# Kernel tuning notes

Measured on AMD Instinct MI355X. Metric: run time of the kernel, lower is better.

Reference implementation:

```python
import jax, jax.numpy as jnp
import numpy as np

N_Q = 5000
MEM = 50
KDIM = 50
VDIM = 200
FC = 50
B = 2048
S = 200


def setup_inputs() -> dict:
    key = jax.random.key(0)
    ks = jax.random.split(key, 14)
    inp = {}
    inp["q_data"] = jax.random.randint(ks[0], (B, S), 0, N_Q, dtype=jnp.int64)
    inp["qa_data"] = jax.random.randint(ks[1], (B, S), 0, 2 * N_Q, dtype=jnp.int64)
    # learned parameters (kaiming-ish random init)
    inp["q_embed_w"] = jax.random.normal(ks[2], (N_Q + 1, KDIM), jnp.float32) * 0.2
    inp["qa_embed_w"] = jax.random.normal(ks[3], (2 * N_Q + 1, VDIM), jnp.float32) * 0.1
    inp["key_memory"] = jax.random.normal(ks[4], (MEM, KDIM), jnp.float32) * 0.2
    inp["init_value_memory"] = jax.random.normal(ks[5], (MEM, VDIM), jnp.float32) * 0.1
    # DKVMN write gates: erase (sigmoid) and add (tanh) transforms of qa embedding
    inp["erase_w"] = jax.random.normal(ks[6], (VDIM, VDIM), jnp.float32) * 0.1
    inp["erase_b"] = jnp.zeros((VDIM,), jnp.float32)
    inp["add_w"] = jax.random.normal(ks[7], (VDIM, VDIM), jnp.float32) * 0.1
    inp["add_b"] = jnp.zeros((VDIM,), jnp.float32)
    # prediction MLP: Linear(VDIM+KDIM -> FC), Tanh, Linear(FC -> 1)
    inp["pred_w1"] = jax.random.normal(ks[8], (VDIM + KDIM, FC), jnp.float32) * 0.1
    inp["pred_b1"] = jnp.zeros((FC,), jnp.float32)
    inp["pred_w2"] = jax.random.normal(ks[9], (FC, 1), jnp.float32) * 0.2
    inp["pred_b2"] = jnp.zeros((1,), jnp.float32)
    return inp


def _dkvmn_forward(q_data, qa_data, q_embed_w, qa_embed_w, key_memory,
                   init_value_memory, erase_w, erase_b, add_w, add_b,
                   pred_w1, pred_b1, pred_w2, pred_b2):
    q_emb = q_embed_w[q_data]    # [B, S, KDIM]
    qa_emb = qa_embed_w[qa_data]  # [B, S, VDIM]
    batch = q_data.shape[0]
    Mv0 = jnp.broadcast_to(init_value_memory, (batch, MEM, VDIM))

    def step(Mv, xs):
        q_t, qa_t = xs  # [B, KDIM], [B, VDIM]
        # attention over memory slots
        w = jax.nn.softmax(q_t @ key_memory.T, axis=-1)          # [B, MEM]
        read = jnp.einsum('bm,bmv->bv', w, Mv)                    # [B, VDIM]
        h = jnp.tanh(jnp.concatenate([read, q_t], -1) @ pred_w1 + pred_b1)
        p = jax.nn.sigmoid((h @ pred_w2 + pred_b2)[:, 0])         # [B]
        # erase/add write
        e = jax.nn.sigmoid(qa_t @ erase_w + erase_b)              # [B, VDIM]
        a = jnp.tanh(qa_t @ add_w + add_b)                        # [B, VDIM]
        Mv_new = Mv * (1.0 - w[:, :, None] * e[:, None, :]) + w[:, :, None] * a[:, None, :]
        return Mv_new, p

    xs = (jnp.swapaxes(q_emb, 0, 1), jnp.swapaxes(qa_emb, 0, 1))  # time-major
    _, preds = jax.lax.scan(step, Mv0, xs)                        # [S, B]
    return preds.T                                                # [B, S]


def reference(q_data, qa_data, q_embed_w, qa_embed_w, key_memory,
              init_value_memory, erase_w, erase_b, add_w, add_b,
              pred_w1, pred_b1, pred_w2, pred_b2):
    preds = _dkvmn_forward(q_data, qa_data, q_embed_w, qa_embed_w, key_memory,
                           init_value_memory, erase_w, erase_b, add_w, add_b,
                           pred_w1, pred_b1, pred_w2, pred_b2)
    zeros = jnp.zeros_like(preds)
    return (preds, zeros, zeros, zeros)
```

## Files before the change

### kernel.cpp

```cpp
#include <hip/hip_runtime.h>
#include <hip/hip_fp16.h>


#define NQ1   5001
#define NQA   10001
#define MEMN  50
#define KD    50
#define VD    200
#define FC    50
#define BB    2048
#define SS    200
#define EA_R  16
#define WHS   32

#define EA_B   626
#define WQ_B   1251
#define PACK_B 8
#define PREP_G (EA_B + WQ_B + PACK_B)

typedef unsigned int   u32;
typedef unsigned short u16;
typedef short    s8v __attribute__((ext_vector_type(8)));
typedef float    f4v __attribute__((ext_vector_type(4)));
typedef _Float16 h2v __attribute__((ext_vector_type(2)));
typedef u32      u4v __attribute__((ext_vector_type(4)));

__device__ __forceinline__ float fast_sigmoid(float x) { return 1.f / (1.f + __expf(-x)); }
__device__ __forceinline__ float fast_tanh(float x) {
    float e2 = __expf(2.f * x);
    return 1.f - 2.f / (e2 + 1.f);
}
__device__ __forceinline__ float bfu16_to_f(u16 u) {
    union { float f; u32 i; } x; x.i = ((u32)u) << 16; return x.f;
}
__device__ __forceinline__ u16 f_to_bfu16(float f) {
    union { float f; u32 i; } x; x.f = f;
    return (u16)((x.i + 0x7fffu + ((x.i >> 16) & 1u)) >> 16);
}
__device__ __forceinline__ h2v u32_to_h2v(u32 u) {
    union { u32 i; h2v h; } x; x.i = u; return x.h;
}
__device__ __forceinline__ u16 f16bits(float f) {
    union { __half h; u16 u; } x; x.h = __float2half(f); return x.u;
}
__device__ __forceinline__ float h16_to_f(u16 u) {
    union { u16 u; __half h; } x; x.u = u; return __half2float(x.h);
}

__global__ __launch_bounds__(256) void prep(
        const float* __restrict__ qemb, const float* __restrict__ km,
        const float* __restrict__ w1,   const float* __restrict__ b1,
        const float* __restrict__ qaemb,
        const float* __restrict__ ew,   const float* __restrict__ ebias,
        const float* __restrict__ aw,   const float* __restrict__ abias,
        float* __restrict__ Wt, u32* __restrict__ Wh, float* __restrict__ Q1,
        u32* __restrict__ EA, u16* __restrict__ W1s,
        float* __restrict__ out_aux) {
    const int tid = threadIdx.x;
    const int blk = blockIdx.x;

    for (size_t i = (size_t)blk * 256 + tid; i < 3ull * BB * SS;
         i += (size_t)PREP_G * 256)
        out_aux[i] = 0.f;

    __shared__ float smem[VD * EA_R];

    if (blk < EA_B) {
        const int r0 = blk * EA_R;
        if (tid < VD) {
            #pragma unroll
            for (int r = 0; r < EA_R; ++r) {
                int row = r0 + r;
                smem[tid * EA_R + r] = (row < NQA) ? qaemb[(size_t)row * VD + tid] : 0.f;
            }
        }
        __syncthreads();
        if (tid >= VD) return;

        float accE[EA_R], accA[EA_R];
        #pragma unroll
        for (int r = 0; r < EA_R; ++r) { accE[r] = 0.f; accA[r] = 0.f; }
        for (int k = 0; k < VD; ++k) {
            float we = ew[k * VD + tid];
            float wa = aw[k * VD + tid];
            #pragma unroll
            for (int r = 0; r < EA_R; ++r) {
                float qv = smem[k * EA_R + r];
                accE[r] = fmaf(qv, we, accE[r]);
                accA[r] = fmaf(qv, wa, accA[r]);
            }
        }
        float be = ebias[tid], ba = abias[tid];
        #pragma unroll
        for (int r = 0; r < EA_R; ++r) {
            int row = r0 + r;
            if (row < NQA) {
                u16 ne16 = f16bits(-fast_sigmoid(accE[r] + be));
                u16 a16  = f16bits(fast_tanh(accA[r] + ba));
                EA[(size_t)row * VD + tid] = (u32)ne16 | ((u32)a16 << 16);
            }
        }
    } else if (blk < EA_B + WQ_B) {
        const int lane = tid & 63;
        const int wv   = tid >> 6;
        const int q    = (blk - EA_B) * 4 + wv;
        const bool qok = q < NQ1;
        float* qrow = smem + wv * 64;
        if (qok && lane < KD) qrow[lane] = qemb[q * KD + lane];
        __syncthreads();
        if (!qok) return;

        float s = -1e30f;
        if (lane < MEMN) {
            s = 0.f;
            #pragma unroll
            for (int k = 0; k < KD; ++k) s = fmaf(qrow[k], km[lane * KD + k], s);
        }
        float mx = s;
        #pragma unroll
        for (int off = 32; off >= 1; off >>= 1) mx = fmaxf(mx, __shfl_xor(mx, off, 64));
        float e = (lane < MEMN) ? __expf(s - mx) : 0.f;
        float sum = e;
        #pragma unroll
        for (int off = 32; off >= 1; off >>= 1) sum += __shfl_xor(sum, off, 64);
        float wv_ = (lane < MEMN) ? (e / sum) : 0.f;
        if (lane < MEMN) Wt[q * MEMN + lane] = wv_;

        float plo = __shfl(wv_, 2 * (lane & 31), 64);
        float phi = __shfl(wv_, 2 * (lane & 31) + 1, 64);
        if (lane < 25) {
            Wh[q * WHS + lane] = (u32)f16bits(plo) | ((u32)f16bits(phi) << 16);
        } else if (lane < WHS) {
            Wh[q * WHS + lane] = 0;
        }

        if (lane < FC) {
            float h = b1[lane];
            #pragma unroll
            for (int k = 0; k < KD; ++k)
                h = fmaf(qrow[k], w1[(VD + k) * FC + lane], h);
            Q1[q * FC + lane] = h;
        }
    } else {
        for (int idx = (blk - EA_B - WQ_B) * 256 + tid; idx < 4 * 7 * 64 * 8;
             idx += PACK_B * 256) {
            int j    = idx & 7;
            int lane = (idx >> 3) & 63;
            int kt   = (idx >> 9) % 7;
            int nt   = idx / 3584;
            int k = kt * 32 + ((lane >> 4) << 3) + j;
            int n = nt * 16 + (lane & 15);
            float v = (k < VD && n < FC) ? w1[k * FC + n] : 0.f;
            W1s[idx] = f_to_bfu16(v);
        }
    }
}

__device__ __forceinline__ void state_step_v(const u4v (&w)[6], u32 w6, u32 ea,
                                             h2v (&mv)[25], float& rdA, float& rdB) {
    h2v nev2 = u32_to_h2v(__builtin_amdgcn_perm(ea, ea, 0x01000100u));
    h2v av2  = u32_to_h2v(__builtin_amdgcn_perm(ea, ea, 0x03020302u));
    rdA = 0.f; rdB = 0.f;
    #pragma unroll
    for (int i = 0; i < 25; i += 2) {
        u32 wu0 = (i < 24) ? w[i >> 2][i & 3] : w6;
        h2v w0 = u32_to_h2v(wu0);
#if __has_builtin(__builtin_amdgcn_fdot2)
        rdA = __builtin_amdgcn_fdot2(w0, mv[i], rdA, false);
#else
        rdA = fmaf((float)w0.x, (float)mv[i].x,
              fmaf((float)w0.y, (float)mv[i].y, rdA));
#endif
        mv[i] = __builtin_elementwise_fma(
            w0, __builtin_elementwise_fma(nev2, mv[i], av2), mv[i]);
        if (i + 1 < 25) {
            h2v w1p = u32_to_h2v(w[(i + 1) >> 2][(i + 1) & 3]);
#if __has_builtin(__builtin_amdgcn_fdot2)
            rdB = __builtin_amdgcn_fdot2(w1p, mv[i + 1], rdB, false);
#else
            rdB = fmaf((float)w1p.x, (float)mv[i + 1].x,
                  fmaf((float)w1p.y, (float)mv[i + 1].y, rdB));
#endif
            mv[i + 1] = __builtin_elementwise_fma(
                w1p, __builtin_elementwise_fma(nev2, mv[i + 1], av2), mv[i + 1]);
        }
    }
}

__global__ __launch_bounds__(128) void dkvmn_state(
        const int* __restrict__ qd, const int* __restrict__ qad,
        const u32* __restrict__ Wh, const u32* __restrict__ EA,
        const float* __restrict__ ivm, u16* __restrict__ READ) {
    const int tid  = threadIdx.x;
    const int lane = tid & 63;
    const int wid  = tid >> 6;
    const int blk  = blockIdx.x;
    const int b    = blk >> 1;
    const int role = (blk & 1) * 2 + wid;
    const int base = b * SS;

    __shared__ int qs[SS], qas[SS];
    for (int i = tid; i < SS; i += 128) {
        qs[i]  = qd[base + i];
        qas[i] = qad[base + i];
    }
    __syncthreads();

    if (role < 3) {
        const int v = role * 64 + lane;

        h2v mv[25];
        #pragma unroll
        for (int i = 0; i < 25; ++i) {
            mv[i].x = (_Float16)ivm[(2 * i) * VD + v];
            mv[i].y = (_Float16)ivm[(2 * i + 1) * VD + v];
        }

        int q0  = qs[0];  asm volatile("" : "+v"(q0));
        int qw  = qs[1];  asm volatile("" : "+v"(qw));
        int qw2 = qs[2];  asm volatile("" : "+v"(qw2));
        int qa2 = qas[2];
        u32 ea_c = EA[(size_t)qas[0] * VD + v];
        u32 ea_n = EA[(size_t)qas[1] * VD + v];

        u4v wA[6]; u32 wA6;
        {
            const u32* rp = Wh + (size_t)q0 * WHS;
            #pragma unroll
            for (int j = 0; j < 6; ++j) wA[j] = *(const u4v*)(rp + j * 4);
            wA6 = rp[24];
        }

        for (int t = 0; t < SS; ++t) {
            int t3 = t + 3; t3 = (t3 < SS) ? t3 : (SS - 1);
            int qnew  = qs[t3];  asm volatile("" : "+v"(qnew));
            int qanew = qas[t3];

            u32 ea_f = EA[(size_t)qa2 * VD + v];

            float rdA, rdB;
            state_step_v(wA, wA6, ea_c, mv, rdA, rdB);
            READ[(size_t)(base + t) * VD + v] = f_to_bfu16(rdA + rdB);

            {
                const u32* rp = Wh + (size_t)qw * WHS;
                #pragma unroll
                for (int j = 0; j < 6; ++j) wA[j] = *(const u4v*)(rp + j * 4);
                wA6 = rp[24];
            }

            qw = qw2; qw2 = qnew; qa2 = qanew;
            ea_c = ea_n; ea_n = ea_f;
        }
    } else {
        const int v8  = lane & 7;
        const int grp = lane >> 3;
        const int v   = 192 + v8;

        h2v mv4[4];
        #pragma unroll
        for (int j = 0; j < 4; ++j) {
            int p = grp * 4 + j;
            if (p < 25) {
                mv4[j].x = (_Float16)ivm[(2 * p) * VD + v];
                mv4[j].y = (_Float16)ivm[(2 * p + 1) * VD + v];
            } else {
                mv4[j].x = (_Float16)0.f;
                mv4[j].y = (_Float16)0.f;
            }
        }

        int q0 = qs[0], q1 = qs[1];
        u32 ea_c = EA[(size_t)qas[0] * VD + v];
        u32 ea_n = EA[(size_t)qas[1] * VD + v];
        u4v wq_c = *(const u4v*)(Wh + (size_t)q0 * WHS + grp * 4);
        u4v wq_n = *(const u4v*)(Wh + (size_t)q1 * WHS + grp * 4);

        for (int t = 0; t < SS; ++t) {
            int tn = t + 2; tn = (tn < SS) ? tn : (SS - 1);
            int q_nn  = qs[tn];
            int qa_nn = qas[tn];
            u32 ea_nn = EA[(size_t)qa_nn * VD + v];
            u4v wq_nn = *(const u4v*)(Wh + (size_t)q_nn * WHS + grp * 4);

            h2v nev2 = u32_to_h2v(__builtin_amdgcn_perm(ea_c, ea_c, 0x01000100u));
            h2v av2  = u32_to_h2v(__builtin_amdgcn_perm(ea_c, ea_c, 0x03020302u));

            float rd = 0.f;
            #pragma unroll
            for (int j = 0; j < 4; ++j) {
                h2v w2 = u32_to_h2v(wq_c[j]);
#if __has_builtin(__builtin_amdgcn_fdot2)
                rd = __builtin_amdgcn_fdot2(w2, mv4[j], rd, false);
#else
                rd = fmaf((float)w2.x, (float)mv4[j].x,
                     fmaf((float)w2.y, (float)mv4[j].y, rd));
#endif
                mv4[j] = __builtin_elementwise_fma(
                    w2, __builtin_elementwise_fma(nev2, mv4[j], av2), mv4[j]);
            }
            rd += __shfl_xor(rd, 8, 64);
            rd += __shfl_xor(rd, 16, 64);
            rd += __shfl_xor(rd, 32, 64);
            if (grp == 0)
                READ[(size_t)(base + t) * VD + v] = f_to_bfu16(rd);

            ea_c = ea_n; ea_n = ea_nn;
            wq_c = wq_n; wq_n = wq_nn;
        }
    }
}

__global__ __launch_bounds__(256) void mlp_pred(
        const u16* __restrict__ RD, const int* __restrict__ qd,
        const float* __restrict__ Q1tab, const u16* __restrict__ W1s,
        const float* __restrict__ w2, const float* __restrict__ b2,
        float* __restrict__ out) {
    const int tid  = threadIdx.x;
    const int lane = tid & 63;
    const int wv   = tid >> 6;
    const int strip = blockIdx.x * 4 + wv;
    const int row0  = strip * 16;

    const int mrow = lane & 15;
    const int quad = lane >> 4;

    s8v a[7];
    {
        const u16* arow = RD + (size_t)(row0 + mrow) * VD + quad * 8;
        #pragma unroll
        for (int kt = 0; kt < 7; ++kt)
            a[kt] = *(const s8v*)(arow + kt * 32);
    }

    const float b2f = b2[0];
    float pf[4] = {0.f, 0.f, 0.f, 0.f};

    #pragma unroll
    for (int nt = 0; nt < 4; ++nt) {
        s8v bfr[7];
        #pragma unroll
        for (int kt = 0; kt < 7; ++kt)
            bfr[kt] = *(const s8v*)(W1s + (((nt * 7 + kt) * 64) + lane) * 8);

        f4v acc = {0.f, 0.f, 0.f, 0.f};
        #pragma unroll
        for (int kt = 0; kt < 7; ++kt)
            acc = __builtin_amdgcn_mfma_f32_16x16x32_bf16(a[kt], bfr[kt], acc, 0, 0, 0);

        const int f = nt * 16 + mrow;
        const float w2f = (f < FC) ? w2[f] : 0.f;
        #pragma unroll
        for (int r = 0; r < 4; ++r) {
            int row = row0 + quad * 4 + r;
            float h = acc[r] + Q1tab[qd[row] * FC + f];
            pf[r] = fmaf(fast_tanh(h), w2f, pf[r]);
        }
    }

    #pragma unroll
    for (int r = 0; r < 4; ++r) {
        float s = pf[r];
        s += __shfl_xor(s, 1, 64);
        s += __shfl_xor(s, 2, 64);
        s += __shfl_xor(s, 4, 64);
        s += __shfl_xor(s, 8, 64);
        if (mrow == 0)
            out[row0 + quad * 4 + r] = fast_sigmoid(s + b2f);
    }
}

__global__ void dkvmn_main(const int* __restrict__ qd, const int* __restrict__ qad,
                           const float* __restrict__ Wtab, const float* __restrict__ Q1tab,
                           const u32* __restrict__ EA,
                           const float* __restrict__ ivm,
                           const float* __restrict__ w1,
                           const float* __restrict__ w2,
                           const float* __restrict__ b2,
                           float* __restrict__ out) {
    const int tid  = threadIdx.x;
    const int b    = blockIdx.x;
    const int v    = tid;
    const int lane = tid & 63;
    const int wv   = tid >> 6;

    __shared__ alignas(16) float read_lds[4 * 52];
    __shared__ alignas(16) float part_lds[4 * 52];

    float mv[MEMN];
    if (v < VD) {
        #pragma unroll
        for (int m = 0; m < MEMN; ++m) mv[m] = ivm[m * VD + v];
    }
    float w1r[50];
    if (lane < FC) {
        #pragma unroll
        for (int i = 0; i < 50; ++i) w1r[i] = w1[(wv * 50 + i) * FC + lane];
    } else {
        #pragma unroll
        for (int i = 0; i < 50; ++i) w1r[i] = 0.f;
    }
    const float w2f = (tid < FC) ? w2[tid] : 0.f;
    const float b2f = b2[0];

    const int* qrow_i  = qd  + b * SS;
    const int* qarow_i = qad + b * SS;
    const int jchunk = v / 50;
    const int wslot  = jchunk * 52 + (v - jchunk * 50);

    for (int t = 0; t < SS; ++t) {
        const int q  = __builtin_amdgcn_readfirstlane(qrow_i[t]);
        const int qa = __builtin_amdgcn_readfirstlane(qarow_i[t]);
        const float* wrow = Wtab + q * MEMN;

        u32 ea = 0;
        if (v < VD) ea = EA[(size_t)qa * VD + v];
        float ne = h16_to_f((u16)(ea & 0xffffu));
        float av = h16_to_f((u16)(ea >> 16));

        if (v < VD) {
            float rd0 = 0.f, rd1 = 0.f;
            #pragma unroll
            for (int m = 0; m < MEMN; m += 2) {
                float wm0 = wrow[m], wm1 = wrow[m + 1];
                rd0 = fmaf(wm0, mv[m], rd0);
                mv[m] = fmaf(wm0, fmaf(ne, mv[m], av), mv[m]);
                rd1 = fmaf(wm1, mv[m + 1], rd1);
                mv[m + 1] = fmaf(wm1, fmaf(ne, mv[m + 1], av), mv[m + 1]);
            }
            read_lds[wslot] = rd0 + rd1;
        }
        __syncthreads();

        float part = 0.f;
        {
            const float* rlc = read_lds + wv * 52;
            #pragma unroll
            for (int i = 0; i < 48; i += 4) {
                float4 x = *(const float4*)(rlc + i);
                part = fmaf(x.x, w1r[i],     part);
                part = fmaf(x.y, w1r[i + 1], part);
                part = fmaf(x.z, w1r[i + 2], part);
                part = fmaf(x.w, w1r[i + 3], part);
            }
            part = fmaf(rlc[48], w1r[48], part);
            part = fmaf(rlc[49], w1r[49], part);
        }
        if (lane < FC) part_lds[wv * 52 + lane] = part;
        __syncthreads();

        if (wv == 0) {
            float pf = 0.f;
            if (lane < FC) {
                float h = part_lds[lane] + part_lds[52 + lane] +
                          part_lds[104 + lane] + part_lds[156 + lane] +
                          Q1tab[q * FC + lane];
                pf = fast_tanh(h) * w2f;
            }
            #pragma unroll
            for (int off = 32; off >= 1; off >>= 1) pf += __shfl_xor(pf, off, 64);
            if (lane == 0) out[b * SS + t] = fast_sigmoid(pf + b2f);
        }
    }
}

extern "C" void kernel_launch(void* const* d_in, const int* in_sizes, int n_in,
                              void* d_out, int out_size, void* d_ws, size_t ws_size,
                              hipStream_t stream) {
    const int* qd  = (const int*)d_in[0];
    const int* qad = (const int*)d_in[1];
    const float* qemb  = (const float*)d_in[2];
    const float* qaemb = (const float*)d_in[3];
    const float* km    = (const float*)d_in[4];
    const float* ivm   = (const float*)d_in[5];
    const float* ew    = (const float*)d_in[6];
    const float* eb    = (const float*)d_in[7];
    const float* aw    = (const float*)d_in[8];
    const float* ab    = (const float*)d_in[9];
    const float* w1    = (const float*)d_in[10];
    const float* b1    = (const float*)d_in[11];
    const float* w2    = (const float*)d_in[12];
    const float* b2    = (const float*)d_in[13];
    float* out = (float*)d_out;
    (void)in_sizes; (void)n_in; (void)out_size;

    char* ws = (char*)d_ws;
    float* Wt  = (float*)(ws);
    float* Q1  = (float*)(ws + 1000448);
    u32*   EA  = (u32*)  (ws + 2000896);
    u16*   W1s = (u16*)  (ws + 10001920);
    u32*   Wh  = (u32*)  (ws + 10034688);
    u16*   RD  = (u16*)  (ws + 10675200);
    const size_t need = 10675200ull + 163840000ull + 512ull;

    prep<<<PREP_G, 256, 0, stream>>>(qemb, km, w1, b1, qaemb, ew, eb, aw, ab,
                                     Wt, Wh, Q1, EA, W1s, out + (size_t)BB * SS);

    if (ws_size >= need) {
        dkvmn_state<<<BB * 2, 128, 0, stream>>>(qd, qad, Wh, EA, ivm, RD);
        mlp_pred<<<(BB * SS) / 64, 256, 0, stream>>>(RD, qd, Q1, W1s, w2, b2, out);
    } else {
        dkvmn_main<<<BB, 256, 0, stream>>>(qd, qad, Wt, Q1, EA, ivm, w1, w2, b2, out);
    }
}
```

Baseline: 507.3 us.

## Stage attention-weight rows into double-buffered LDS in groups of 16 steps

In the recurrent state kernel, each wave used to fetch the per-step attention-weight row from global memory, prefetching only one to two steps ahead. Now both waves of the block load the rows for the next 16 time steps into a double-buffered shared-memory tile while the current group runs. A barrier separates each group, and the inner loop reads the row from LDS. The goal is to take global-load latency off the serial time-step chain, at the cost of one block barrier per group and extra LDS traffic.

```diff
diff --git a/kernel.cpp b/kernel.cpp
--- a/kernel.cpp
+++ b/kernel.cpp
@@ -17,6 +17,9 @@
 #define WQ_B   1251
 #define PACK_B 8
 #define PREP_G (EA_B + WQ_B + PACK_B)
+
+#define WGRP  16
+#define NG    13
 
 typedef unsigned int   u32;
 typedef unsigned short u16;
@@ -200,12 +203,31 @@
     const int base = b * SS;
 
     __shared__ int qs[SS], qas[SS];
+    __shared__ u32 wlds[2][WGRP][WHS];
+
     for (int i = tid; i < SS; i += 128) {
         qs[i]  = qd[base + i];
         qas[i] = qad[base + i];
     }
     __syncthreads();
 
+    const int wword = tid & 31;
+    const int wsub  = tid >> 5;
+
+    {
+        u32 w0s[4];
+        #pragma unroll
+        for (int r = 0; r < 4; ++r) {
+            int s = r * 4 + wsub;
+            int q = qs[(s < SS) ? s : (SS - 1)];
+            w0s[r] = Wh[(size_t)q * WHS + wword];
+        }
+        #pragma unroll
+        for (int r = 0; r < 4; ++r)
+            wlds[0][r * 4 + wsub][wword] = w0s[r];
+    }
+    __syncthreads();
+
     if (role < 3) {
         const int v = role * 64 + lane;
 
@@ -216,41 +238,48 @@
             mv[i].y = (_Float16)ivm[(2 * i + 1) * VD + v];
         }
 
-        int q0  = qs[0];  asm volatile("" : "+v"(q0));
-        int qw  = qs[1];  asm volatile("" : "+v"(qw));
-        int qw2 = qs[2];  asm volatile("" : "+v"(qw2));
-        int qa2 = qas[2];
         u32 ea_c = EA[(size_t)qas[0] * VD + v];
         u32 ea_n = EA[(size_t)qas[1] * VD + v];
 
-        u4v wA[6]; u32 wA6;
-        {
-            const u32* rp = Wh + (size_t)q0 * WHS;
-            #pragma unroll
-            for (int j = 0; j < 6; ++j) wA[j] = *(const u4v*)(rp + j * 4);
-            wA6 = rp[24];
-        }
-
-        for (int t = 0; t < SS; ++t) {
-            int t3 = t + 3; t3 = (t3 < SS) ? t3 : (SS - 1);
-            int qnew  = qs[t3];  asm volatile("" : "+v"(qnew));
-            int qanew = qas[t3];
-
-            u32 ea_f = EA[(size_t)qa2 * VD + v];
-
-            float rdA, rdB;
-            state_step_v(wA, wA6, ea_c, mv, rdA, rdB);
-            READ[(size_t)(base + t) * VD + v] = f_to_bfu16(rdA + rdB);
-
-            {
-                const u32* rp = Wh + (size_t)qw * WHS;
+        for (int g = 0; g < NG; ++g) {
+            u32 wstage[4];
+            const bool do_stage = (g + 1 < NG);
+            if (do_stage) {
+                int s0 = (g + 1) * WGRP;
                 #pragma unroll
-                for (int j = 0; j < 6; ++j) wA[j] = *(const u4v*)(rp + j * 4);
-                wA6 = rp[24];
-            }
-
-            qw = qw2; qw2 = qnew; qa2 = qanew;
-            ea_c = ea_n; ea_n = ea_f;
+                for (int r = 0; r < 4; ++r) {
+                    int s = s0 + r * 4 + wsub;
+                    int q = qs[(s < SS) ? s : (SS - 1)];
+                    wstage[r] = Wh[(size_t)q * WHS + wword];
+                }
+            }
+
+            const int nS = (g == NG - 1) ? (SS - WGRP * (NG - 1)) : WGRP;
+            #pragma unroll 4
+            for (int s = 0; s < nS; ++s) {
+                const int t = g * WGRP + s;
+                const u32* wrow = &wlds[g & 1][s][0];
+                u4v wr[6];
+                #pragma unroll
+                for (int j = 0; j < 6; ++j) wr[j] = *(const u4v*)(wrow + j * 4);
+                u32 wr6 = wrow[24];
+
+                int t2 = t + 2; t2 = (t2 < SS) ? t2 : (SS - 1);
+                u32 ea_f = EA[(size_t)qas[t2] * VD + v];
+
+                float rdA, rdB;
+                state_step_v(wr, wr6, ea_c, mv, rdA, rdB);
+                READ[(size_t)(base + t) * VD + v] = f_to_bfu16(rdA + rdB);
+
+                ea_c = ea_n; ea_n = ea_f;
+            }
+
+            if (do_stage) {
+                #pragma unroll
+                for (int r = 0; r < 4; ++r)
+                    wlds[(g + 1) & 1][r * 4 + wsub][wword] = wstage[r];
+            }
+            __syncthreads();
         }
     } else {
         const int v8  = lane & 7;
@@ -270,43 +299,62 @@
             }
         }
 
-        int q0 = qs[0], q1 = qs[1];
         u32 ea_c = EA[(size_t)qas[0] * VD + v];
         u32 ea_n = EA[(size_t)qas[1] * VD + v];
-        u4v wq_c = *(const u4v*)(Wh + (size_t)q0 * WHS + grp * 4);
-        u4v wq_n = *(const u4v*)(Wh + (size_t)q1 * WHS + grp * 4);
-
-        for (int t = 0; t < SS; ++t) {
-            int tn = t + 2; tn = (tn < SS) ? tn : (SS - 1);
-            int q_nn  = qs[tn];
-            int qa_nn = qas[tn];
-            u32 ea_nn = EA[(size_t)qa_nn * VD + v];
-            u4v wq_nn = *(const u4v*)(Wh + (size_t)q_nn * WHS + grp * 4);
-
-            h2v nev2 = u32_to_h2v(__builtin_amdgcn_perm(ea_c, ea_c, 0x01000100u));
-            h2v av2  = u32_to_h2v(__builtin_amdgcn_perm(ea_c, ea_c, 0x03020302u));
-
-            float rd = 0.f;
-            #pragma unroll
-            for (int j = 0; j < 4; ++j) {
-                h2v w2 = u32_to_h2v(wq_c[j]);
+
+        for (int g = 0; g < NG; ++g) {
+            u32 wstage[4];
+            const bool do_stage = (g + 1 < NG);
+            if (do_stage) {
+                int s0 = (g + 1) * WGRP;
+                #pragma unroll
+                for (int r = 0; r < 4; ++r) {
+                    int s = s0 + r * 4 + wsub;
+                    int q = qs[(s < SS) ? s : (SS - 1)];
+                    wstage[r] = Wh[(size_t)q * WHS + wword];
+                }
+            }
+
+            const int nS = (g == NG - 1) ? (SS - WGRP * (NG - 1)) : WGRP;
+            #pragma unroll 4
+            for (int s = 0; s < nS; ++s) {
+                const int t = g * WGRP + s;
+                u4v wq = *(const u4v*)(&wlds[g & 1][s][grp * 4]);
+
+                int t2 = t + 2; t2 = (t2 < SS) ? t2 : (SS - 1);
+                u32 ea_f = EA[(size_t)qas[t2] * VD + v];
+
+                h2v nev2 = u32_to_h2v(__builtin_amdgcn_perm(ea_c, ea_c, 0x01000100u));
+                h2v av2  = u32_to_h2v(__builtin_amdgcn_perm(ea_c, ea_c, 0x03020302u));
+
+                float rd = 0.f;
+                #pragma unroll
+                for (int j = 0; j < 4; ++j) {
+                    h2v w2 = u32_to_h2v(wq[j]);
 #if __has_builtin(__builtin_amdgcn_fdot2)
-                rd = __builtin_amdgcn_fdot2(w2, mv4[j], rd, false);
+                    rd = __builtin_amdgcn_fdot2(w2, mv4[j], rd, false);
 #else
-                rd = fmaf((float)w2.x, (float)mv4[j].x,
-                     fmaf((float)w2.y, (float)mv4[j].y, rd));
+                    rd = fmaf((float)w2.x, (float)mv4[j].x,
+                         fmaf((float)w2.y, (float)mv4[j].y, rd));
 #endif
-                mv4[j] = __builtin_elementwise_fma(
-                    w2, __builtin_elementwise_fma(nev2, mv4[j], av2), mv4[j]);
-            }
-            rd += __shfl_xor(rd, 8, 64);
-            rd += __shfl_xor(rd, 16, 64);
-            rd += __shfl_xor(rd, 32, 64);
-            if (grp == 0)
-                READ[(size_t)(base + t) * VD + v] = f_to_bfu16(rd);
-
-            ea_c = ea_n; ea_n = ea_nn;
-            wq_c = wq_n; wq_n = wq_nn;
+                    mv4[j] = __builtin_elementwise_fma(
+                        w2, __builtin_elementwise_fma(nev2, mv4[j], av2), mv4[j]);
+                }
+                rd += __shfl_xor(rd, 8, 64);
+                rd += __shfl_xor(rd, 16, 64);
+                rd += __shfl_xor(rd, 32, 64);
+                if (grp == 0)
+                    READ[(size_t)(base + t) * VD + v] = f_to_bfu16(rd);
+
+                ea_c = ea_n; ea_n = ea_f;
+            }
+
+            if (do_stage) {
+                #pragma unroll
+                for (int r = 0; r < 4; ++r)
+                    wlds[(g + 1) & 1][r * 4 + wsub][wword] = wstage[r];
+            }
+            __syncthreads();
         }
     }
 }
```

After: 463.3 us. 8.7% less time.

## Stage per-step attention weight rows through LDS in groups of eight

Applied to the files above, without the earlier changes.

Replaces the per-timestep global loads of the Wh attention-weight row with a cooperative staging scheme. Each wave fetches the rows for the next eight timesteps one group ahead, with each lane loading a single word. At the end of a group it writes them into a per-wave LDS window. Each step then reads its row from LDS into a double-buffered register set. The aim is to take global memory latency off the serial recurrence, at the cost of more LDS traffic, extra registers and more complicated index bookkeeping.

```diff
diff --git a/kernel.cpp b/kernel.cpp
--- a/kernel.cpp
+++ b/kernel.cpp
@@ -17,6 +17,8 @@
 #define WQ_B   1251
 #define PACK_B 8
 #define PREP_G (EA_B + WQ_B + PACK_B)
+
+#define WG    8
 
 typedef unsigned int   u32;
 typedef unsigned short u16;
@@ -200,6 +202,8 @@
     const int base = b * SS;
 
     __shared__ int qs[SS], qas[SS];
+    __shared__ u32 win[2][WG][WHS];
+
     for (int i = tid; i < SS; i += 128) {
         qs[i]  = qd[base + i];
         qas[i] = qad[base + i];
@@ -207,7 +211,9 @@
     __syncthreads();
 
     if (role < 3) {
-        const int v = role * 64 + lane;
+        const int v    = role * 64 + lane;
+        const int word = lane & 31;
+        const int half = lane >> 5;
 
         h2v mv[25];
         #pragma unroll
@@ -216,41 +222,77 @@
             mv[i].y = (_Float16)ivm[(2 * i + 1) * VD + v];
         }
 
-        int q0  = qs[0];  asm volatile("" : "+v"(q0));
-        int qw  = qs[1];  asm volatile("" : "+v"(qw));
-        int qw2 = qs[2];  asm volatile("" : "+v"(qw2));
-        int qa2 = qas[2];
+        u32 wst[4];
+        {
+            int qg0[4];
+            #pragma unroll
+            for (int i = 0; i < 4; ++i) qg0[i] = qs[i * 2 + half];
+            #pragma unroll
+            for (int i = 0; i < 4; ++i)
+                wst[i] = Wh[(size_t)qg0[i] * WHS + word];
+            #pragma unroll
+            for (int i = 0; i < 4; ++i)
+                win[wid][i * 2 + half][word] = wst[i];
+        }
+        int qstage[4];
+        #pragma unroll
+        for (int i = 0; i < 4; ++i) qstage[i] = qs[WG + i * 2 + half];
+
+        u4v wrb[2][6]; u32 wrb6[2];
+        {
+            const u32* wp = &win[wid][0][0];
+            #pragma unroll
+            for (int j = 0; j < 6; ++j) wrb[0][j] = *(const u4v*)(wp + j * 4);
+            wrb6[0] = wp[24];
+        }
+
+        int qa2 = qas[2], qa3 = qas[3];
         u32 ea_c = EA[(size_t)qas[0] * VD + v];
         u32 ea_n = EA[(size_t)qas[1] * VD + v];
 
-        u4v wA[6]; u32 wA6;
-        {
-            const u32* rp = Wh + (size_t)q0 * WHS;
-            #pragma unroll
-            for (int j = 0; j < 6; ++j) wA[j] = *(const u4v*)(rp + j * 4);
-            wA6 = rp[24];
-        }
-
-        for (int t = 0; t < SS; ++t) {
-            int t3 = t + 3; t3 = (t3 < SS) ? t3 : (SS - 1);
-            int qnew  = qs[t3];  asm volatile("" : "+v"(qnew));
-            int qanew = qas[t3];
-
-            u32 ea_f = EA[(size_t)qa2 * VD + v];
-
-            float rdA, rdB;
-            state_step_v(wA, wA6, ea_c, mv, rdA, rdB);
-            READ[(size_t)(base + t) * VD + v] = f_to_bfu16(rdA + rdB);
-
-            {
-                const u32* rp = Wh + (size_t)qw * WHS;
-                #pragma unroll
-                for (int j = 0; j < 6; ++j) wA[j] = *(const u4v*)(rp + j * 4);
-                wA6 = rp[24];
-            }
-
-            qw = qw2; qw2 = qnew; qa2 = qanew;
-            ea_c = ea_n; ea_n = ea_f;
+        for (int g = 0; g < SS / WG; ++g) {
+            #pragma unroll
+            for (int s = 0; s < WG; ++s) {
+                const int t   = g * WG + s;
+                const int cur = s & 1;
+                const int nxt = cur ^ 1;
+
+                if (s == 0) {
+                    #pragma unroll
+                    for (int i = 0; i < 4; ++i)
+                        wst[i] = Wh[(size_t)qstage[i] * WHS + word];
+                }
+                if (s == WG - 1) {
+                    #pragma unroll
+                    for (int i = 0; i < 4; ++i)
+                        win[wid][i * 2 + half][word] = wst[i];
+                    #pragma unroll
+                    for (int i = 0; i < 4; ++i) {
+                        int idx = (g + 2) * WG + i * 2 + half;
+                        idx = (idx < SS) ? idx : (SS - 1);
+                        qstage[i] = qs[idx];
+                    }
+                }
+
+                {
+                    const u32* wp = &win[wid][(s + 1) & (WG - 1)][0];
+                    #pragma unroll
+                    for (int j = 0; j < 6; ++j)
+                        wrb[nxt][j] = *(const u4v*)(wp + j * 4);
+                    wrb6[nxt] = wp[24];
+                }
+
+                u32 ea_f = EA[(size_t)qa2 * VD + v];
+                int t4 = t + 4; t4 = (t4 < SS) ? t4 : (SS - 1);
+                int qa_nn = qas[t4];
+
+                float rdA, rdB;
+                state_step_v(wrb[cur], wrb6[cur], ea_c, mv, rdA, rdB);
+                READ[(size_t)(base + t) * VD + v] = f_to_bfu16(rdA + rdB);
+
+                qa2 = qa3; qa3 = qa_nn;
+                ea_c = ea_n; ea_n = ea_f;
+            }
         }
     } else {
         const int v8  = lane & 7;
```

After: 447.3 us. -11.8%, faster.
